# Optimization experiments

Measured on AMD Instinct MI355X. Metric: run time of the kernel, lower is better.

## Reference

```python
import jax, jax.numpy as jnp
import numpy as np

N, C_IN, C_OUT = 8192, 128, 128
BN_EPS = 1e-5
EDGE_PROB = 0.004  # avg degree ~33


def setup_inputs() -> dict:
    key = jax.random.key(0)
    k1, k2, k3, k4, k5, k6 = jax.random.split(key, 6)
    node_features = jax.random.normal(k1, (N, C_IN), dtype=jnp.float32)
    # binary dense adjacency (rand fill, thresholded to ~avg degree 33)
    adjacency_matrix = (jax.random.uniform(k2, (N, N)) < EDGE_PROB).astype(jnp.float32)
    s = 1.0 / np.sqrt(C_IN)
    W_n = jax.random.uniform(k3, (C_OUT, C_IN), jnp.float32, -s, s)
    b_n = jax.random.uniform(k4, (C_OUT,), jnp.float32, -s, s)
    W_c = jax.random.uniform(k5, (C_OUT, C_IN), jnp.float32, -s, s)
    b_c = jax.random.uniform(k6, (C_OUT,), jnp.float32, -s, s)
    gamma = jnp.ones((C_OUT,), jnp.float32)
    beta = jnp.zeros((C_OUT,), jnp.float32)
    return {"node_features": node_features, "adjacency_matrix": adjacency_matrix,
            "W_n": W_n, "b_n": b_n, "W_c": W_c, "b_c": b_c,
            "gamma": gamma, "beta": beta}


def reference(node_features, adjacency_matrix, W_n, b_n, W_c, b_c, gamma, beta):
    # mean aggregation: degrees from row-sums (as in the torch code), agg = A.T @ X / deg
    deg = adjacency_matrix.sum(axis=1, keepdims=True)          # [N,1]
    deg = jnp.where(deg == 0, jnp.ones_like(deg), deg)
    agg = (adjacency_matrix.T @ node_features) / deg           # [N,C_in]
    h = agg @ W_n.T + b_n + node_features @ W_c.T + b_c        # [N,C_out]
    # BatchNorm1d, training-mode batch stats (biased variance)
    mu = h.mean(axis=0)
    var = ((h - mu) ** 2).mean(axis=0)
    h_norm = (h - mu) * jax.lax.rsqrt(var + BN_EPS)
    return jax.nn.relu(gamma * h_norm + beta)
```

## Files before the change

kernel.cpp:

```cpp
#include <hip/hip_runtime.h>
#include <stdint.h>

#define NN 8192
#define CC 128
#define BN_EPS 1e-5f

__device__ inline unsigned short f2bf(float f) {
    unsigned int u = __float_as_uint(f);
    unsigned int r = (u + 0x7fffu + ((u >> 16) & 1u)) >> 16;
    return (unsigned short)r;
}
__device__ inline float bf2f(unsigned short s) {
    return __uint_as_float(((unsigned int)s) << 16);
}

__global__ __launch_bounds__(256, 2) void k1_spmm(
        const float* __restrict__ A, const float* __restrict__ X,
        float* __restrict__ aggU, float* __restrict__ deg) {
    __shared__ float acc[128 * 128];
    const int tid  = threadIdx.x;
    const int lane = tid & 63;
    const int wave = tid >> 6;
    const int i0   = blockIdx.x * 128;
    const int jbase = blockIdx.y * 1024 + wave * 256;

    for (int t = tid; t < 128 * 128; t += 256) acc[t] = 0.0f;
    __syncthreads();

    for (int jj = 0; jj < 256; jj += 4) {
        float2 a[4]; float xa[4], xb[4];
        #pragma unroll
        for (int u = 0; u < 4; ++u) {
            int j = jbase + jj + u;
            a[u]  = *reinterpret_cast<const float2*>(A + (size_t)j * NN + i0 + lane * 2);
            xa[u] = X[j * CC + lane];
            xb[u] = X[j * CC + 64 + lane];
        }
        #pragma unroll
        for (int u = 0; u < 4; ++u) {
            int j = jbase + jj + u;
            unsigned long long m0 = __ballot(a[u].x != 0.0f);
            unsigned long long m1 = __ballot(a[u].y != 0.0f);
            int cnt = __popcll(m0) + __popcll(m1);
            if (cnt) {
                if (lane == 0) atomicAdd(&deg[j], (float)cnt);
                while (m0) {
                    int b = __builtin_ctzll(m0); m0 &= m0 - 1;
                    int row = b * 2;
                    atomicAdd(&acc[row * 128 + lane],      xa[u]);
                    atomicAdd(&acc[row * 128 + 64 + lane], xb[u]);
                }
                while (m1) {
                    int b = __builtin_ctzll(m1); m1 &= m1 - 1;
                    int row = b * 2 + 1;
                    atomicAdd(&acc[row * 128 + lane],      xa[u]);
                    atomicAdd(&acc[row * 128 + 64 + lane], xb[u]);
                }
            }
        }
    }
    __syncthreads();
    float* aggBase = aggU + (size_t)i0 * CC;
    for (int t = tid; t < 128 * 128; t += 256) atomicAdd(&aggBase[t], acc[t]);
}

__global__ __launch_bounds__(256, 2) void k2_gemm(
        const float* __restrict__ aggU, const float* __restrict__ deg,
        const float* __restrict__ X,
        const float* __restrict__ Wn, const float* __restrict__ bn,
        const float* __restrict__ Wc, const float* __restrict__ bc,
        float* __restrict__ h, float* __restrict__ bsum, float* __restrict__ bsq) {
    __shared__ unsigned short WtN[128 * 128];
    __shared__ unsigned short WtC[128 * 128];
    const int tid = threadIdx.x;
    for (int idx = tid; idx < 128 * 128; idx += 256) {
        int c = idx >> 7, k = idx & 127;
        WtN[k * 128 + c] = f2bf(Wn[idx]);
        WtC[k * 128 + c] = f2bf(Wc[idx]);
    }
    __syncthreads();
    const int c  = tid & 127;
    const int rg = tid >> 7;
    const int i0 = blockIdx.x * 16 + rg * 8;

    float accN[8], accC[8];
    #pragma unroll
    for (int r = 0; r < 8; ++r) { accN[r] = 0.0f; accC[r] = 0.0f; }

    for (int k = 0; k < 128; k += 4) {
        float4 ar[8], xr[8];
        #pragma unroll
        for (int r = 0; r < 8; ++r) {
            ar[r] = *reinterpret_cast<const float4*>(&aggU[(size_t)(i0 + r) * CC + k]);
            xr[r] = *reinterpret_cast<const float4*>(&X[(size_t)(i0 + r) * CC + k]);
        }
        #pragma unroll
        for (int kk = 0; kk < 4; ++kk) {
            float wn = bf2f(WtN[(k + kk) * 128 + c]);
            float wc = bf2f(WtC[(k + kk) * 128 + c]);
            #pragma unroll
            for (int r = 0; r < 8; ++r) {
                float av = (&ar[r].x)[kk];
                float xv = (&xr[r].x)[kk];
                accN[r] = fmaf(av, wn, accN[r]);
                accC[r] = fmaf(xv, wc, accC[r]);
            }
        }
    }

    const float bnc = bn[c], bcc = bc[c];
    float sp = 0.0f, sq = 0.0f;
    #pragma unroll
    for (int r = 0; r < 8; ++r) {
        float d  = deg[i0 + r];
        float rd = (d == 0.0f) ? 1.0f : (1.0f / d);
        float hv = accN[r] * rd + accC[r] + bnc + bcc;
        h[(size_t)(i0 + r) * CC + c] = hv;
        sp += hv; sq += hv * hv;
    }
    __syncthreads();
    float* red = reinterpret_cast<float*>(WtN);
    red[rg * 128 + c]       = sp;
    red[256 + rg * 128 + c] = sq;
    __syncthreads();
    if (rg == 0) {
        atomicAdd(&bsum[c], red[c] + red[128 + c]);
        atomicAdd(&bsq[c],  red[256 + c] + red[384 + c]);
    }
}

__global__ __launch_bounds__(256) void k4_bn(
        const float* __restrict__ h, const float* __restrict__ bsum,
        const float* __restrict__ bsq, const float* __restrict__ gamma,
        const float* __restrict__ beta, float* __restrict__ out) {
    const int idx = (blockIdx.x * 256 + threadIdx.x) * 4;
    const int c0  = idx & 127;
    float4 hv = *reinterpret_cast<const float4*>(h + idx);
    float4 s4 = *reinterpret_cast<const float4*>(bsum + c0);
    float4 q4 = *reinterpret_cast<const float4*>(bsq + c0);
    float4 g4 = *reinterpret_cast<const float4*>(gamma + c0);
    float4 b4 = *reinterpret_cast<const float4*>(beta + c0);
    const float invN = 1.0f / 8192.0f;
    float4 o;
    const float* hp = &hv.x; const float* sp = &s4.x; const float* qp = &q4.x;
    const float* gp = &g4.x; const float* bp = &b4.x; float* op = &o.x;
    #pragma unroll
    for (int jj = 0; jj < 4; ++jj) {
        float mu  = sp[jj] * invN;
        float var = qp[jj] * invN - mu * mu;
        float sc  = gp[jj] * rsqrtf(var + BN_EPS);
        float v   = (hp[jj] - mu) * sc + bp[jj];
        op[jj] = v > 0.0f ? v : 0.0f;
    }
    *reinterpret_cast<float4*>(out + idx) = o;
}

extern "C" void kernel_launch(void* const* d_in, const int* in_sizes, int n_in,
                              void* d_out, int out_size, void* d_ws, size_t ws_size,
                              hipStream_t stream) {
    const float* X     = (const float*)d_in[0];
    const float* A     = (const float*)d_in[1];
    const float* Wn    = (const float*)d_in[2];
    const float* bn    = (const float*)d_in[3];
    const float* Wc    = (const float*)d_in[4];
    const float* bc    = (const float*)d_in[5];
    const float* gamma = (const float*)d_in[6];
    const float* beta  = (const float*)d_in[7];
    float* out = (float*)d_out;

    char* ws = (char*)d_ws;
    float* aggU = (float*)(ws);
    float* deg  = (float*)(ws + 4194304);
    float* bsum = (float*)(ws + 4227072);
    float* bsq  = (float*)(ws + 4227584);
    float* h    = (float*)(ws + 4228096);

    hipMemsetAsync(d_ws, 0, 4228096, stream);

    k1_spmm<<<dim3(64, 8), 256, 0, stream>>>(A, X, aggU, deg);
    k2_gemm<<<512, 256, 0, stream>>>(aggU, deg, X, Wn, bn, Wc, bc, h, bsum, bsq);
    k4_bn<<<1024, 256, 0, stream>>>(h, bsum, bsq, gamma, beta, out);
}
```

Baseline: 535.7 us.

## Software-pipeline SpMM and GEMM loads with double-buffered registers and wider A loads

The SpMM kernel now reads A as float4, with each wave covering two adjacency rows per load (half-wave per row). It double-buffers 8-row batches in registers so global loads of the next batch overlap the ballot/atomic processing of the current one. The GEMM kernel similarly prefetches the next k-slice of aggU/X while computing the current one, and loads the weights with float4 during the transpose. This targets exposed memory latency at the cost of higher register pressure, which could lower occupancy under launch_bounds(256,2).

Result: no change. 529.1 us (-1.2%).

```diff
diff --git a/kernel.cpp b/kernel.cpp
--- a/kernel.cpp
+++ b/kernel.cpp
@@ -13,6 +13,58 @@
 __device__ inline float bf2f(unsigned short s) {
     return __uint_as_float(((unsigned int)s) << 16);
 }
+
+__device__ __forceinline__ void process_pair(
+        float4 a, float xa0, float xb0, float xa1, float xb1,
+        int j0, float* __restrict__ acc, float* __restrict__ deg, int lane) {
+    unsigned long long m0 = __ballot(a.x != 0.0f);
+    unsigned long long m1 = __ballot(a.y != 0.0f);
+    unsigned long long m2 = __ballot(a.z != 0.0f);
+    unsigned long long m3 = __ballot(a.w != 0.0f);
+    if ((m0 | m1 | m2 | m3) == 0ull) return;
+    const unsigned long long LO = 0xffffffffull;
+    int c0 = __popcll(m0 & LO) + __popcll(m1 & LO) + __popcll(m2 & LO) + __popcll(m3 & LO);
+    int c1 = __popcll(m0 >> 32) + __popcll(m1 >> 32) + __popcll(m2 >> 32) + __popcll(m3 >> 32);
+    if (lane == 0 && c0) atomicAdd(&deg[j0], (float)c0);
+    if (lane == 1 && c1) atomicAdd(&deg[j0 + 1], (float)c1);
+    unsigned long long m[4] = {m0, m1, m2, m3};
+    #pragma unroll
+    for (int comp = 0; comp < 4; ++comp) {
+        unsigned int lo = (unsigned int)m[comp];
+        while (lo) {
+            int b = __builtin_ctz(lo); lo &= lo - 1;
+            int il = 4 * b + comp;
+            atomicAdd(&acc[il * 128 + lane],      xa0);
+            atomicAdd(&acc[il * 128 + 64 + lane], xb0);
+        }
+        unsigned int hi = (unsigned int)(m[comp] >> 32);
+        while (hi) {
+            int b = __builtin_ctz(hi); hi &= hi - 1;
+            int il = 4 * b + comp;
+            atomicAdd(&acc[il * 128 + lane],      xa1);
+            atomicAdd(&acc[il * 128 + 64 + lane], xb1);
+        }
+    }
+}
+
+#define LOADB(a_, xa_, xb_, j0_) do {                                          \
+    const float* Ap_ = A + (size_t)((j0_) + (lane >> 5)) * NN + i0 + ((lane & 31) << 2); \
+    _Pragma("unroll")                                                          \
+    for (int u = 0; u < 4; ++u)                                                \
+        a_[u] = *reinterpret_cast<const float4*>(Ap_ + (size_t)(2 * u) * NN);  \
+    _Pragma("unroll")                                                          \
+    for (int r = 0; r < 8; ++r) {                                              \
+        xa_[r] = X[((j0_) + r) * CC + lane];                                   \
+        xb_[r] = X[((j0_) + r) * CC + 64 + lane];                              \
+    }                                                                          \
+} while (0)
+
+#define PROCB(a_, xa_, xb_, j0_) do {                                          \
+    _Pragma("unroll")                                                          \
+    for (int u = 0; u < 4; ++u)                                                \
+        process_pair(a_[u], xa_[2 * u], xb_[2 * u], xa_[2 * u + 1],            \
+                     xb_[2 * u + 1], (j0_) + 2 * u, acc, deg, lane);           \
+} while (0)
 
 __global__ __launch_bounds__(256, 2) void k1_spmm(
         const float* __restrict__ A, const float* __restrict__ X,
@@ -27,38 +79,18 @@
     for (int t = tid; t < 128 * 128; t += 256) acc[t] = 0.0f;
     __syncthreads();
 
-    for (int jj = 0; jj < 256; jj += 4) {
-        float2 a[4]; float xa[4], xb[4];
-        #pragma unroll
-        for (int u = 0; u < 4; ++u) {
-            int j = jbase + jj + u;
-            a[u]  = *reinterpret_cast<const float2*>(A + (size_t)j * NN + i0 + lane * 2);
-            xa[u] = X[j * CC + lane];
-            xb[u] = X[j * CC + 64 + lane];
-        }
-        #pragma unroll
-        for (int u = 0; u < 4; ++u) {
-            int j = jbase + jj + u;
-            unsigned long long m0 = __ballot(a[u].x != 0.0f);
-            unsigned long long m1 = __ballot(a[u].y != 0.0f);
-            int cnt = __popcll(m0) + __popcll(m1);
-            if (cnt) {
-                if (lane == 0) atomicAdd(&deg[j], (float)cnt);
-                while (m0) {
-                    int b = __builtin_ctzll(m0); m0 &= m0 - 1;
-                    int row = b * 2;
-                    atomicAdd(&acc[row * 128 + lane],      xa[u]);
-                    atomicAdd(&acc[row * 128 + 64 + lane], xb[u]);
-                }
-                while (m1) {
-                    int b = __builtin_ctzll(m1); m1 &= m1 - 1;
-                    int row = b * 2 + 1;
-                    atomicAdd(&acc[row * 128 + lane],      xa[u]);
-                    atomicAdd(&acc[row * 128 + 64 + lane], xb[u]);
-                }
-            }
-        }
-    }
+    float4 a0[4], a1[4];
+    float xa0[8], xb0[8], xa1[8], xb1[8];
+
+    LOADB(a0, xa0, xb0, jbase);
+    for (int it2 = 0; it2 < 16; ++it2) {
+        int j0 = jbase + it2 * 16;
+        LOADB(a1, xa1, xb1, j0 + 8);
+        PROCB(a0, xa0, xb0, j0);
+        if (it2 < 15) LOADB(a0, xa0, xb0, j0 + 16);
+        PROCB(a1, xa1, xb1, j0 + 8);
+    }
+
     __syncthreads();
     float* aggBase = aggU + (size_t)i0 * CC;
     for (int t = tid; t < 128 * 128; t += 256) atomicAdd(&aggBase[t], acc[t]);
@@ -73,10 +105,18 @@
     __shared__ unsigned short WtN[128 * 128];
     __shared__ unsigned short WtC[128 * 128];
     const int tid = threadIdx.x;
-    for (int idx = tid; idx < 128 * 128; idx += 256) {
-        int c = idx >> 7, k = idx & 127;
-        WtN[k * 128 + c] = f2bf(Wn[idx]);
-        WtC[k * 128 + c] = f2bf(Wc[idx]);
+    for (int idx = tid * 4; idx < 128 * 128; idx += 1024) {
+        float4 wn4 = *reinterpret_cast<const float4*>(Wn + idx);
+        float4 wc4 = *reinterpret_cast<const float4*>(Wc + idx);
+        int c = idx >> 7, k0 = idx & 127;
+        WtN[(k0 + 0) * 128 + c] = f2bf(wn4.x);
+        WtN[(k0 + 1) * 128 + c] = f2bf(wn4.y);
+        WtN[(k0 + 2) * 128 + c] = f2bf(wn4.z);
+        WtN[(k0 + 3) * 128 + c] = f2bf(wn4.w);
+        WtC[(k0 + 0) * 128 + c] = f2bf(wc4.x);
+        WtC[(k0 + 1) * 128 + c] = f2bf(wc4.y);
+        WtC[(k0 + 2) * 128 + c] = f2bf(wc4.z);
+        WtC[(k0 + 3) * 128 + c] = f2bf(wc4.w);
     }
     __syncthreads();
     const int c  = tid & 127;
@@ -87,25 +127,35 @@
     #pragma unroll
     for (int r = 0; r < 8; ++r) { accN[r] = 0.0f; accC[r] = 0.0f; }
 
-    for (int k = 0; k < 128; k += 4) {
-        float4 ar[8], xr[8];
-        #pragma unroll
-        for (int r = 0; r < 8; ++r) {
-            ar[r] = *reinterpret_cast<const float4*>(&aggU[(size_t)(i0 + r) * CC + k]);
-            xr[r] = *reinterpret_cast<const float4*>(&X[(size_t)(i0 + r) * CC + k]);
-        }
-        #pragma unroll
-        for (int kk = 0; kk < 4; ++kk) {
-            float wn = bf2f(WtN[(k + kk) * 128 + c]);
-            float wc = bf2f(WtC[(k + kk) * 128 + c]);
-            #pragma unroll
-            for (int r = 0; r < 8; ++r) {
-                float av = (&ar[r].x)[kk];
-                float xv = (&xr[r].x)[kk];
-                accN[r] = fmaf(av, wn, accN[r]);
-                accC[r] = fmaf(xv, wc, accC[r]);
-            }
-        }
+    float4 ar[8], xr[8], an[8], xn[8];
+
+#define LOADK(ab_, xb_, k_) do {                                               \
+    _Pragma("unroll")                                                          \
+    for (int r = 0; r < 8; ++r) {                                              \
+        ab_[r] = *reinterpret_cast<const float4*>(&aggU[(size_t)(i0 + r) * CC + (k_)]); \
+        xb_[r] = *reinterpret_cast<const float4*>(&X[(size_t)(i0 + r) * CC + (k_)]);    \
+    }                                                                          \
+} while (0)
+
+#define COMPK(ab_, xb_, k_) do {                                               \
+    _Pragma("unroll")                                                          \
+    for (int kk = 0; kk < 4; ++kk) {                                           \
+        float wn_ = bf2f(WtN[((k_) + kk) * 128 + c]);                          \
+        float wc_ = bf2f(WtC[((k_) + kk) * 128 + c]);                          \
+        _Pragma("unroll")                                                      \
+        for (int r = 0; r < 8; ++r) {                                          \
+            accN[r] = fmaf((&ab_[r].x)[kk], wn_, accN[r]);                     \
+            accC[r] = fmaf((&xb_[r].x)[kk], wc_, accC[r]);                     \
+        }                                                                      \
+    }                                                                          \
+} while (0)
+
+    LOADK(ar, xr, 0);
+    for (int k = 0; k < 128; k += 8) {
+        LOADK(an, xn, k + 4);
+        COMPK(ar, xr, k);
+        if (k + 8 < 128) LOADK(ar, xr, k + 8);
+        COMPK(an, xn, k + 4);
     }
 
     const float bnc = bn[c], bcc = bc[c];
```
